# Kernel tuning notes

Hardware: AMD Instinct MI355X
Metric: run time of the kernel (lower is better)

Reference implementation:

```python
import jax, jax.numpy as jnp
import numpy as np

H = 64  # rnn_hidden_size


def _rnn_seq(x, W_ih, W_hh, b_ih, b_hh):
    """One tanh RNN layer over [B,T,D] -> full output sequence [B,T,H]."""
    pre = jnp.einsum('btd,hd->bth', x, W_ih) + b_ih  # input projection hoisted out of the scan
    h0 = jnp.zeros((x.shape[0], W_hh.shape[0]), x.dtype)
    def step(h, p_t):
        h = jnp.tanh(p_t + h @ W_hh.T + b_hh)
        return h, h
    _, ys = jax.lax.scan(step, h0, jnp.swapaxes(pre, 0, 1))  # scan over time
    return jnp.swapaxes(ys, 0, 1)


def _rnn_last(x, W_ih, W_hh, b_ih, b_hh):
    """One tanh RNN layer, returning only the last hidden state [B,H]."""
    pre = jnp.einsum('btd,hd->bth', x, W_ih) + b_ih
    h0 = jnp.zeros((x.shape[0], W_hh.shape[0]), x.dtype)
    def step(h, p_t):
        return jnp.tanh(p_t + h @ W_hh.T + b_hh), None
    h, _ = jax.lax.scan(step, h0, jnp.swapaxes(pre, 0, 1))
    return h


def setup_inputs() -> dict:
    key = jax.random.key(0)
    ks = jax.random.split(key, 32)
    B, T, D = 128, 4096, 3
    kr = 1.0 / np.sqrt(H)          # PyTorch RNN init bound
    u = lambda kk, shape, b: jax.random.uniform(kk, shape, jnp.float32, -b, b)
    inp = {
        'x': jax.random.normal(ks[0], (B, T, D), jnp.float32),
        'y': jax.random.normal(ks[1], (B, T, D), jnp.float32),
        'z': jax.random.normal(ks[2], (5,), jnp.float32),
        # rnn_empty, layer 0 (in=3) and layer 1 (in=64)
        'e_Wih0': u(ks[3], (H, D), kr), 'e_Whh0': u(ks[4], (H, H), kr),
        'e_bih0': u(ks[5], (H,), kr),  'e_bhh0': u(ks[6], (H,), kr),
        'e_Wih1': u(ks[7], (H, H), kr), 'e_Whh1': u(ks[8], (H, H), kr),
        'e_bih1': u(ks[9], (H,), kr),  'e_bhh1': u(ks[10], (H,), kr),
        # rnn_occupied
        'o_Wih0': u(ks[11], (H, D), kr), 'o_Whh0': u(ks[12], (H, H), kr),
        'o_bih0': u(ks[13], (H,), kr),  'o_bhh0': u(ks[14], (H,), kr),
        'o_Wih1': u(ks[15], (H, H), kr), 'o_Whh1': u(ks[16], (H, H), kr),
        'o_bih1': u(ks[17], (H,), kr),  'o_bhh1': u(ks[18], (H,), kr),
        # heads: fce/fco (64->2), fc1 (9->64), fc2 (64->5)
        'fce_w': u(ks[19], (2, H), kr), 'fce_b': u(ks[20], (2,), kr),
        'fco_w': u(ks[21], (2, H), kr), 'fco_b': u(ks[22], (2,), kr),
        'fc1_w': u(ks[23], (64, 9), 1.0 / np.sqrt(9)), 'fc1_b': u(ks[24], (64,), 1.0 / np.sqrt(9)),
        'fc2_w': u(ks[25], (5, 64), kr), 'fc2_b': u(ks[26], (5,), kr),
    }
    return inp


def reference(x, y, z,
              e_Wih0, e_Whh0, e_bih0, e_bhh0, e_Wih1, e_Whh1, e_bih1, e_bhh1,
              o_Wih0, o_Whh0, o_bih0, o_bhh0, o_Wih1, o_Whh1, o_bih1, o_bhh1,
              fce_w, fce_b, fco_w, fco_b, fc1_w, fc1_b, fc2_w, fc2_b):
    # two 2-layer tanh RNNs; last-timestep output of layer 2 == final hidden of layer 2
    hx = _rnn_last(_rnn_seq(x, e_Wih0, e_Whh0, e_bih0, e_bhh0),
                   e_Wih1, e_Whh1, e_bih1, e_bhh1)            # [B,H]
    hy = _rnn_last(_rnn_seq(y, o_Wih0, o_Whh0, o_bih0, o_bhh0),
                   o_Wih1, o_Whh1, o_bih1, o_bhh1)            # [B,H]
    e = hx @ fce_w.T + fce_b                                  # [B,2]
    o = hy @ fco_w.T + fco_b                                  # [B,2]
    zz = jnp.concatenate([e[0], o[0], z])                     # [9]
    h = jax.nn.relu(zz @ fc1_w.T + fc1_b)                     # [64]
    return h @ fc2_w.T + fc2_b                                # [5]
```

## Files before the change

### kernel.cpp

```cpp
#include <hip/hip_runtime.h>

#define T 4096
#define EP 8
#define RING 32
#define NEP (T / EP + 2)

__device__ __forceinline__ float fast_tanh(float x) {
    float e = __expf(2.0f * x);
    float r = __builtin_amdgcn_rcpf(e + 1.0f);
    return fmaf(-2.0f, r, 1.0f);
}

__device__ __forceinline__ float lane_bcast(float v, int j) {
    return __uint_as_float(__builtin_amdgcn_readlane(__float_as_uint(v), j));
}

__global__ void prep_kernel(const float* __restrict__ x, const float* __restrict__ y,
                            const float* __restrict__ eW, const float* __restrict__ ebi,
                            const float* __restrict__ ebh,
                            const float* __restrict__ oW, const float* __restrict__ obi,
                            const float* __restrict__ obh,
                            float* __restrict__ pre)
{
    int idx = blockIdx.x * blockDim.x + threadIdx.x;
    int i = idx & 63;
    int t = (idx >> 6) & (T - 1);
    int s = idx >> 18;
    const float* in = s ? y : x;
    const float* W  = s ? oW : eW;
    const float* bi = s ? obi : ebi;
    const float* bh = s ? obh : ebh;
    float v = bi[i] + bh[i]
            + W[i*3+0]*in[t*3+0] + W[i*3+1]*in[t*3+1] + W[i*3+2]*in[t*3+2];
    pre[idx] = v;
}

__global__ __launch_bounds__(192, 1) void seq_kernel(
    const float* __restrict__ pre,
    const float* __restrict__ eWhh0, const float* __restrict__ eWih1,
    const float* __restrict__ eWhh1, const float* __restrict__ ebih1,
    const float* __restrict__ ebhh1,
    const float* __restrict__ oWhh0, const float* __restrict__ oWih1,
    const float* __restrict__ oWhh1, const float* __restrict__ obih1,
    const float* __restrict__ obhh1,
    float* __restrict__ hlast)
{
    const int s    = blockIdx.x;
    const int wv   = threadIdx.x >> 6;
    const int lane = threadIdx.x & 63;

    __shared__ __align__(16) float h0ring[RING][64];
    __shared__ __align__(16) float qring[RING][64];

    const float* p = pre + s * T * 64;

    if (wv == 0) {
        const float* Whh0 = s ? oWhh0 : eWhh0;
        float w0[64];
#pragma unroll
        for (int j = 0; j < 64; ++j) w0[j] = Whh0[lane * 64 + j];

        float hp = 0.f;
        float pc[EP], pn[EP];
#pragma unroll
        for (int i = 0; i < EP; ++i) pc[i] = p[i * 64 + lane];

        for (int k = 0; k < NEP; ++k) {
            const int base = k * EP;
#pragma unroll
            for (int i = 0; i < EP; ++i) {
                int t = base + EP + i;
                pn[i] = (t < T) ? p[t * 64 + lane] : 0.f;
            }
            if (base < T) {
#pragma unroll
                for (int i = 0; i < EP; ++i) {
                    float aa[4] = { pc[i], 0.f, 0.f, 0.f };
#pragma unroll
                    for (int jb = 0; jb < 64; jb += 8) {
                        float hj[8];
#pragma unroll
                        for (int u = 0; u < 8; ++u) hj[u] = lane_bcast(hp, jb + u);
#pragma unroll
                        for (int u = 0; u < 8; ++u)
                            aa[u & 3] = fmaf(w0[jb + u], hj[u], aa[u & 3]);
                    }
                    hp = fast_tanh((aa[0] + aa[1]) + (aa[2] + aa[3]));
                    h0ring[(base + i) & (RING - 1)][lane] = hp;
                }
            }
#pragma unroll
            for (int i = 0; i < EP; ++i) pc[i] = pn[i];
            __syncthreads();
        }
    } else if (wv == 1) {
        const float* Wih1 = s ? oWih1 : eWih1;
        const float  b1   = s ? (obih1[lane] + obhh1[lane])
                              : (ebih1[lane] + ebhh1[lane]);
        float wi[64];
#pragma unroll
        for (int j = 0; j < 64; ++j) wi[j] = Wih1[lane * 64 + j];

        for (int k = 0; k < NEP; ++k) {
            const int base = k * EP - EP;
            if (base >= 0 && base < T) {
#pragma unroll
                for (int i = 0; i < EP; ++i) {
                    const int t = base + i;
                    const float4* hv = (const float4*)h0ring[t & (RING - 1)];
                    float q[4] = { b1, 0.f, 0.f, 0.f };
#pragma unroll
                    for (int j4 = 0; j4 < 16; ++j4) {
                        float4 u = hv[j4];
                        q[0] = fmaf(wi[4*j4+0], u.x, q[0]);
                        q[1] = fmaf(wi[4*j4+1], u.y, q[1]);
                        q[2] = fmaf(wi[4*j4+2], u.z, q[2]);
                        q[3] = fmaf(wi[4*j4+3], u.w, q[3]);
                    }
                    qring[t & (RING - 1)][lane] = (q[0] + q[1]) + (q[2] + q[3]);
                }
            }
            __syncthreads();
        }
    } else {
        const float* Whh1 = s ? oWhh1 : eWhh1;
        float w1[64];
#pragma unroll
        for (int j = 0; j < 64; ++j) w1[j] = Whh1[lane * 64 + j];

        float hp = 0.f;
        for (int k = 0; k < NEP; ++k) {
            const int base = k * EP - 2 * EP;
            if (base >= 0) {
                float qb[EP];
#pragma unroll
                for (int i = 0; i < EP; ++i)
                    qb[i] = qring[(base + i) & (RING - 1)][lane];
#pragma unroll
                for (int i = 0; i < EP; ++i) {
                    float cc[4] = { qb[i], 0.f, 0.f, 0.f };
#pragma unroll
                    for (int jb = 0; jb < 64; jb += 8) {
                        float hj[8];
#pragma unroll
                        for (int u = 0; u < 8; ++u) hj[u] = lane_bcast(hp, jb + u);
#pragma unroll
                        for (int u = 0; u < 8; ++u)
                            cc[u & 3] = fmaf(w1[jb + u], hj[u], cc[u & 3]);
                    }
                    hp = fast_tanh((cc[0] + cc[1]) + (cc[2] + cc[3]));
                }
            }
            __syncthreads();
        }
        hlast[s * 64 + lane] = hp;
    }
}

__global__ void head_kernel(const float* __restrict__ hlast,
                            const float* __restrict__ z,
                            const float* __restrict__ fce_w, const float* __restrict__ fce_b,
                            const float* __restrict__ fco_w, const float* __restrict__ fco_b,
                            const float* __restrict__ fc1_w, const float* __restrict__ fc1_b,
                            const float* __restrict__ fc2_w, const float* __restrict__ fc2_b,
                            float* __restrict__ out)
{
    const int lane = threadIdx.x;
    __shared__ float zz[9];
    __shared__ float hh[64];

    if (lane < 2) {
        float sacc = fce_b[lane];
        for (int j = 0; j < 64; ++j) sacc += fce_w[lane * 64 + j] * hlast[j];
        zz[lane] = sacc;
    } else if (lane < 4) {
        int r = lane - 2;
        float sacc = fco_b[r];
        for (int j = 0; j < 64; ++j) sacc += fco_w[r * 64 + j] * hlast[64 + j];
        zz[lane] = sacc;
    } else if (lane < 9) {
        zz[lane] = z[lane - 4];
    }
    __syncthreads();

    float sacc = fc1_b[lane];
#pragma unroll
    for (int j = 0; j < 9; ++j) sacc += fc1_w[lane * 9 + j] * zz[j];
    hh[lane] = fmaxf(sacc, 0.f);
    __syncthreads();

    if (lane < 5) {
        float o = fc2_b[lane];
        for (int i = 0; i < 64; ++i) o += fc2_w[lane * 64 + i] * hh[i];
        out[lane] = o;
    }
}

extern "C" void kernel_launch(void* const* d_in, const int* in_sizes, int n_in,
                              void* d_out, int out_size, void* d_ws, size_t ws_size,
                              hipStream_t stream)
{
    const float* x      = (const float*)d_in[0];
    const float* y      = (const float*)d_in[1];
    const float* z      = (const float*)d_in[2];
    const float* e_Wih0 = (const float*)d_in[3];
    const float* e_Whh0 = (const float*)d_in[4];
    const float* e_bih0 = (const float*)d_in[5];
    const float* e_bhh0 = (const float*)d_in[6];
    const float* e_Wih1 = (const float*)d_in[7];
    const float* e_Whh1 = (const float*)d_in[8];
    const float* e_bih1 = (const float*)d_in[9];
    const float* e_bhh1 = (const float*)d_in[10];
    const float* o_Wih0 = (const float*)d_in[11];
    const float* o_Whh0 = (const float*)d_in[12];
    const float* o_bih0 = (const float*)d_in[13];
    const float* o_bhh0 = (const float*)d_in[14];
    const float* o_Wih1 = (const float*)d_in[15];
    const float* o_Whh1 = (const float*)d_in[16];
    const float* o_bih1 = (const float*)d_in[17];
    const float* o_bhh1 = (const float*)d_in[18];
    const float* fce_w  = (const float*)d_in[19];
    const float* fce_b  = (const float*)d_in[20];
    const float* fco_w  = (const float*)d_in[21];
    const float* fco_b  = (const float*)d_in[22];
    const float* fc1_w  = (const float*)d_in[23];
    const float* fc1_b  = (const float*)d_in[24];
    const float* fc2_w  = (const float*)d_in[25];
    const float* fc2_b  = (const float*)d_in[26];

    float* pre   = (float*)d_ws;
    float* hlast = pre + 2 * T * 64;
    float* out   = (float*)d_out;

    prep_kernel<<<(2 * T * 64) / 256, 256, 0, stream>>>(
        x, y, e_Wih0, e_bih0, e_bhh0, o_Wih0, o_bih0, o_bhh0, pre);

    seq_kernel<<<2, 192, 0, stream>>>(
        pre,
        e_Whh0, e_Wih1, e_Whh1, e_bih1, e_bhh1,
        o_Whh0, o_Wih1, o_Whh1, o_bih1, o_bhh1,
        hlast);

    head_kernel<<<1, 64, 0, stream>>>(
        hlast, z, fce_w, fce_b, fco_w, fco_b, fc1_w, fc1_b, fc2_w, fc2_b, out);
}
```

Before: 1.196 ms.

## Fuse layer-1 input projection into layer-0 recurrence wave, drop middle wave

The layer-1 input projection (Wih1·h0) moves into the layer-0 recurrence wave, which reuses the readlane-broadcast h values it already computes. This removes the h0 shared-memory ring and the separate middle wave, so the block shrinks from three waves to two. The cost is an extra 64 FMAs per step on the serial critical path of wave 0, plus double the weight registers in that wave. Inline-asm pins keep the weights in VGPRs.

```diff
diff --git a/kernel.cpp b/kernel.cpp
--- a/kernel.cpp
+++ b/kernel.cpp
@@ -14,6 +14,8 @@
 __device__ __forceinline__ float lane_bcast(float v, int j) {
     return __uint_as_float(__builtin_amdgcn_readlane(__float_as_uint(v), j));
 }
+
+#define PIN(x) asm volatile("" : "+v"(x))
 
 __global__ void prep_kernel(const float* __restrict__ x, const float* __restrict__ y,
                             const float* __restrict__ eW, const float* __restrict__ ebi,
@@ -35,7 +37,7 @@
     pre[idx] = v;
 }
 
-__global__ __launch_bounds__(192, 1) void seq_kernel(
+__global__ __launch_bounds__(128, 1) void seq_kernel(
     const float* __restrict__ pre,
     const float* __restrict__ eWhh0, const float* __restrict__ eWih1,
     const float* __restrict__ eWhh1, const float* __restrict__ ebih1,
@@ -49,16 +51,22 @@
     const int wv   = threadIdx.x >> 6;
     const int lane = threadIdx.x & 63;
 
-    __shared__ __align__(16) float h0ring[RING][64];
     __shared__ __align__(16) float qring[RING][64];
 
     const float* p = pre + s * T * 64;
 
     if (wv == 0) {
         const float* Whh0 = s ? oWhh0 : eWhh0;
-        float w0[64];
+        const float* Wih1 = s ? oWih1 : eWih1;
+        const float  b1   = s ? (obih1[lane] + obhh1[lane])
+                              : (ebih1[lane] + ebhh1[lane]);
+        float w0[64], wi[64];
 #pragma unroll
         for (int j = 0; j < 64; ++j) w0[j] = Whh0[lane * 64 + j];
+#pragma unroll
+        for (int j = 0; j < 64; ++j) wi[j] = Wih1[lane * 64 + j];
+#pragma unroll
+        for (int j = 0; j < 64; ++j) { PIN(w0[j]); PIN(wi[j]); }
 
         float hp = 0.f;
         float pc[EP], pn[EP];
@@ -72,54 +80,33 @@
                 int t = base + EP + i;
                 pn[i] = (t < T) ? p[t * 64 + lane] : 0.f;
             }
-            if (base < T) {
+            if (base <= T) {
 #pragma unroll
                 for (int i = 0; i < EP; ++i) {
-                    float aa[4] = { pc[i], 0.f, 0.f, 0.f };
-#pragma unroll
-                    for (int jb = 0; jb < 64; jb += 8) {
-                        float hj[8];
-#pragma unroll
-                        for (int u = 0; u < 8; ++u) hj[u] = lane_bcast(hp, jb + u);
-#pragma unroll
-                        for (int u = 0; u < 8; ++u)
-                            aa[u & 3] = fmaf(w0[jb + u], hj[u], aa[u & 3]);
+                    const int t = base + i;
+                    if (t <= T) {
+                        float aa[4] = { pc[i], 0.f, 0.f, 0.f };
+                        float qq[4] = { b1,    0.f, 0.f, 0.f };
+#pragma unroll
+                        for (int jb = 0; jb < 64; jb += 8) {
+                            float hj[8];
+#pragma unroll
+                            for (int u = 0; u < 8; ++u) hj[u] = lane_bcast(hp, jb + u);
+#pragma unroll
+                            for (int u = 0; u < 8; ++u) {
+                                aa[u & 3] = fmaf(w0[jb + u], hj[u], aa[u & 3]);
+                                qq[u & 3] = fmaf(wi[jb + u], hj[u], qq[u & 3]);
+                            }
+                        }
+                        qring[(t + RING - 1) & (RING - 1)][lane] =
+                            (qq[0] + qq[1]) + (qq[2] + qq[3]);
+                        if (t < T)
+                            hp = fast_tanh((aa[0] + aa[1]) + (aa[2] + aa[3]));
                     }
-                    hp = fast_tanh((aa[0] + aa[1]) + (aa[2] + aa[3]));
-                    h0ring[(base + i) & (RING - 1)][lane] = hp;
                 }
             }
 #pragma unroll
             for (int i = 0; i < EP; ++i) pc[i] = pn[i];
-            __syncthreads();
-        }
-    } else if (wv == 1) {
-        const float* Wih1 = s ? oWih1 : eWih1;
-        const float  b1   = s ? (obih1[lane] + obhh1[lane])
-                              : (ebih1[lane] + ebhh1[lane]);
-        float wi[64];
-#pragma unroll
-        for (int j = 0; j < 64; ++j) wi[j] = Wih1[lane * 64 + j];
-
-        for (int k = 0; k < NEP; ++k) {
-            const int base = k * EP - EP;
-            if (base >= 0 && base < T) {
-#pragma unroll
-                for (int i = 0; i < EP; ++i) {
-                    const int t = base + i;
-                    const float4* hv = (const float4*)h0ring[t & (RING - 1)];
-                    float q[4] = { b1, 0.f, 0.f, 0.f };
-#pragma unroll
-                    for (int j4 = 0; j4 < 16; ++j4) {
-                        float4 u = hv[j4];
-                        q[0] = fmaf(wi[4*j4+0], u.x, q[0]);
-                        q[1] = fmaf(wi[4*j4+1], u.y, q[1]);
-                        q[2] = fmaf(wi[4*j4+2], u.z, q[2]);
-                        q[3] = fmaf(wi[4*j4+3], u.w, q[3]);
-                    }
-                    qring[t & (RING - 1)][lane] = (q[0] + q[1]) + (q[2] + q[3]);
-                }
-            }
             __syncthreads();
         }
     } else {
@@ -127,11 +114,13 @@
         float w1[64];
 #pragma unroll
         for (int j = 0; j < 64; ++j) w1[j] = Whh1[lane * 64 + j];
+#pragma unroll
+        for (int j = 0; j < 64; ++j) PIN(w1[j]);
 
         float hp = 0.f;
         for (int k = 0; k < NEP; ++k) {
-            const int base = k * EP - 2 * EP;
-            if (base >= 0) {
+            const int base = (k - 2) * EP;
+            if (base >= 0 && base < T) {
                 float qb[EP];
 #pragma unroll
                 for (int i = 0; i < EP; ++i)
@@ -235,7 +224,7 @@
     prep_kernel<<<(2 * T * 64) / 256, 256, 0, stream>>>(
         x, y, e_Wih0, e_bih0, e_bhh0, o_Wih0, o_bih0, o_bhh0, pre);
 
-    seq_kernel<<<2, 192, 0, stream>>>(
+    seq_kernel<<<2, 128, 0, stream>>>(
         pre,
         e_Whh0, e_Wih1, e_Whh1, e_bih1, e_bhh1,
         o_Whh0, o_Wih1, o_Whh1, o_bih1, o_bhh1,
```

Result: slower. 1.338 ms (+11.9%).

## Replace readlane broadcasts with DPP row-rotate chain in recurrent matvecs

Applied to the files above, without the earlier changes.

The recurrent h@W_hh products in both serial RNN waves now rotate the hidden-state register across lanes with a DPP rotate-by-one on each step, instead of reading each of the 64 lanes one at a time via readlane into scalar registers. Weights are pre-permuted per lane to match the rotation order, with the direction found at runtime. This is meant to remove the SGPR round-trip and the scalar/vector dependency stalls of 64 readlanes per timestep. The risk is that DPP row_ror only rotates within 16-lane rows, so a 64-lane rotation may give wrong results. tanh now uses exp2 directly, and the prefetch of the next step's input is clamped rather than predicated.

```diff
diff --git a/kernel.cpp b/kernel.cpp
--- a/kernel.cpp
+++ b/kernel.cpp
@@ -6,14 +6,22 @@
 #define NEP (T / EP + 2)
 
 __device__ __forceinline__ float fast_tanh(float x) {
-    float e = __expf(2.0f * x);
+    float e = __builtin_amdgcn_exp2f(x * 2.8853900817779268f);
     float r = __builtin_amdgcn_rcpf(e + 1.0f);
     return fmaf(-2.0f, r, 1.0f);
 }
 
-__device__ __forceinline__ float lane_bcast(float v, int j) {
-    return __uint_as_float(__builtin_amdgcn_readlane(__float_as_uint(v), j));
-}
+__device__ __forceinline__ int dpp_ror1_i(int x) {
+    return __builtin_amdgcn_update_dpp(x, x, 0x13C, 0xF, 0xF, false);
+}
+
+__device__ __forceinline__ int dpp_dir(int lane) {
+    int r  = dpp_ror1_i(lane);
+    int l0 = __builtin_amdgcn_readfirstlane(r);
+    return (l0 == 1) ? 1 : -1;
+}
+
+#define PIN(x) asm volatile("" : "+v"(x))
 
 __global__ void prep_kernel(const float* __restrict__ x, const float* __restrict__ y,
                             const float* __restrict__ eW, const float* __restrict__ ebi,
@@ -56,9 +64,12 @@
 
     if (wv == 0) {
         const float* Whh0 = s ? oWhh0 : eWhh0;
+        const int d = dpp_dir(lane);
         float w0[64];
 #pragma unroll
-        for (int j = 0; j < 64; ++j) w0[j] = Whh0[lane * 64 + j];
+        for (int k = 0; k < 64; ++k) w0[k] = Whh0[lane * 64 + ((lane + d * k) & 63)];
+#pragma unroll
+        for (int k = 0; k < 64; ++k) PIN(w0[k]);
 
         float hp = 0.f;
         float pc[EP], pn[EP];
@@ -67,30 +78,27 @@
 
         for (int k = 0; k < NEP; ++k) {
             const int base = k * EP;
-#pragma unroll
-            for (int i = 0; i < EP; ++i) {
-                int t = base + EP + i;
-                pn[i] = (t < T) ? p[t * 64 + lane] : 0.f;
+            if (base < T) {
+#pragma unroll
+                for (int i = 0; i < EP; ++i) {
+                    int tt = base + EP + i; tt = (tt < T) ? tt : (T - 1);
+                    pn[i] = p[tt * 64 + lane];
+                }
+#pragma unroll
+                for (int i = 0; i < EP; ++i) {
+                    float a[4] = { pc[i], 0.f, 0.f, 0.f };
+                    int hr = __float_as_int(hp);
+#pragma unroll
+                    for (int k2 = 0; k2 < 64; ++k2) {
+                        a[k2 & 3] = fmaf(w0[k2], __int_as_float(hr), a[k2 & 3]);
+                        if (k2 < 63) hr = dpp_ror1_i(hr);
+                    }
+                    hp = fast_tanh((a[0] + a[1]) + (a[2] + a[3]));
+                    h0ring[(base + i) & (RING - 1)][lane] = hp;
+                }
+#pragma unroll
+                for (int i = 0; i < EP; ++i) pc[i] = pn[i];
             }
-            if (base < T) {
-#pragma unroll
-                for (int i = 0; i < EP; ++i) {
-                    float aa[4] = { pc[i], 0.f, 0.f, 0.f };
-#pragma unroll
-                    for (int jb = 0; jb < 64; jb += 8) {
-                        float hj[8];
-#pragma unroll
-                        for (int u = 0; u < 8; ++u) hj[u] = lane_bcast(hp, jb + u);
-#pragma unroll
-                        for (int u = 0; u < 8; ++u)
-                            aa[u & 3] = fmaf(w0[jb + u], hj[u], aa[u & 3]);
-                    }
-                    hp = fast_tanh((aa[0] + aa[1]) + (aa[2] + aa[3]));
-                    h0ring[(base + i) & (RING - 1)][lane] = hp;
-                }
-            }
-#pragma unroll
-            for (int i = 0; i < EP; ++i) pc[i] = pn[i];
             __syncthreads();
         }
     } else if (wv == 1) {
@@ -100,9 +108,11 @@
         float wi[64];
 #pragma unroll
         for (int j = 0; j < 64; ++j) wi[j] = Wih1[lane * 64 + j];
+#pragma unroll
+        for (int j = 0; j < 64; ++j) PIN(wi[j]);
 
         for (int k = 0; k < NEP; ++k) {
-            const int base = k * EP - EP;
+            const int base = (k - 1) * EP;
             if (base >= 0 && base < T) {
 #pragma unroll
                 for (int i = 0; i < EP; ++i) {
@@ -124,31 +134,31 @@
         }
     } else {
         const float* Whh1 = s ? oWhh1 : eWhh1;
+        const int d = dpp_dir(lane);
         float w1[64];
 #pragma unroll
-        for (int j = 0; j < 64; ++j) w1[j] = Whh1[lane * 64 + j];
+        for (int k = 0; k < 64; ++k) w1[k] = Whh1[lane * 64 + ((lane + d * k) & 63)];
+#pragma unroll
+        for (int k = 0; k < 64; ++k) PIN(w1[k]);
 
         float hp = 0.f;
         for (int k = 0; k < NEP; ++k) {
-            const int base = k * EP - 2 * EP;
-            if (base >= 0) {
+            const int base = (k - 2) * EP;
+            if (base >= 0 && base < T) {
                 float qb[EP];
 #pragma unroll
                 for (int i = 0; i < EP; ++i)
                     qb[i] = qring[(base + i) & (RING - 1)][lane];
 #pragma unroll
                 for (int i = 0; i < EP; ++i) {
-                    float cc[4] = { qb[i], 0.f, 0.f, 0.f };
-#pragma unroll
-                    for (int jb = 0; jb < 64; jb += 8) {
-                        float hj[8];
-#pragma unroll
-                        for (int u = 0; u < 8; ++u) hj[u] = lane_bcast(hp, jb + u);
-#pragma unroll
-                        for (int u = 0; u < 8; ++u)
-                            cc[u & 3] = fmaf(w1[jb + u], hj[u], cc[u & 3]);
+                    float c[4] = { qb[i], 0.f, 0.f, 0.f };
+                    int hr = __float_as_int(hp);
+#pragma unroll
+                    for (int k2 = 0; k2 < 64; ++k2) {
+                        c[k2 & 3] = fmaf(w1[k2], __int_as_float(hr), c[k2 & 3]);
+                        if (k2 < 63) hr = dpp_ror1_i(hr);
                     }
-                    hp = fast_tanh((cc[0] + cc[1]) + (cc[2] + cc[3]));
+                    hp = fast_tanh((c[0] + c[1]) + (c[2] + c[3]));
                 }
             }
             __syncthreads();
```

New measurement: 2.092 ms. 75.0% more time.
